# Performance work log

Hardware: AMD Instinct MI355X
Metric: run time of the kernel (lower is better)

The kernel has to match this reference:

```python
import jax, jax.numpy as jnp
import numpy as np

B, LP, LH, D, H = 32, 1024, 1024, 256, 256

def setup_inputs() -> dict:
    key = jax.random.key(0)
    k1, k2, k3 = jax.random.split(key, 3)
    premises = jax.random.normal(k1, (B, LP, D), dtype=jnp.float32)
    hypotheses = jax.random.normal(k2, (B, LH, D), dtype=jnp.float32)
    W_F = jax.random.normal(k3, (D, H), dtype=jnp.float32) * (1.0 / np.sqrt(D))
    return {"premises": premises, "hypotheses": hypotheses, "W_F": W_F}

def reference(premises, hypotheses, W_F):
    # Tanh-projected features: F_p = tanh(P @ W_F), F_h = tanh(H @ W_F)
    F_p = jnp.tanh(jnp.einsum('bpd,dh->bph', premises, W_F))   # [B,LP,H]
    F_h = jnp.tanh(jnp.einsum('bqd,dh->bqh', hypotheses, W_F)) # [B,LH,H]
    # Alignment scores e_ij = F_p . F_h
    eijs = jnp.einsum('bph,bqh->bpq', F_p, F_h)                # [B,LP,LH]
    # betas: for each premise token, softmax over hypothesis tokens, weighted sum of hypotheses
    betas = jnp.einsum('bpq,bqd->bpd', jax.nn.softmax(eijs, axis=-1), hypotheses)  # [B,LP,D]
    # alphas: for each hypothesis token, softmax over premise tokens, weighted sum of premises
    alphas = jnp.einsum('bqp,bpd->bqd',
                        jax.nn.softmax(jnp.swapaxes(eijs, 1, 2), axis=-1),
                        premises)                                                   # [B,LH,D]
    return betas, alphas
```

## Files before the change

kernel.cpp:

```cpp
#include <hip/hip_runtime.h>

typedef _Float16 f16;
typedef __attribute__((ext_vector_type(4))) _Float16 f16x4;
typedef __attribute__((ext_vector_type(8))) _Float16 f16x8;
typedef __attribute__((ext_vector_type(4))) float f32x4;
typedef __attribute__((ext_vector_type(16))) float f32x16;
typedef unsigned int u32;

#define BB 32
#define LL 1024
#define DD 256

#define VMCNT(N) asm volatile("s_waitcnt vmcnt(" #N ")" ::: "memory")
#define LGKMCNT0 asm volatile("s_waitcnt lgkmcnt(0)" ::: "memory")

__device__ __forceinline__ void async_copy16(const f16* g, f16* l) {
  __builtin_amdgcn_global_load_lds(
      (const __attribute__((address_space(1))) u32*)(const void*)g,
      (__attribute__((address_space(3))) u32*)(void*)l, 16, 0, 0);
}

__device__ __forceinline__ u32 pack_pkrtz(float a, float b) {
  auto pk = __builtin_amdgcn_cvt_pkrtz(a, b);
  u32 w;
  __builtin_memcpy(&w, &pk, 4);
  return w;
}


__global__ __launch_bounds__(256) void w_to_frag(const float* __restrict__ W,
                                                 f16* __restrict__ WtF) {
  __shared__ float T32[256][33];
  const int tid = threadIdx.x;
  const int N = blockIdx.x;
  const int nn = tid & 31, kr = tid >> 5;
#pragma unroll
  for (int p = 0; p < 32; ++p) {
    int k = p * 8 + kr;
    T32[k][nn] = W[(size_t)k * 256 + N * 32 + nn];
  }
  __syncthreads();
  const int wv = tid >> 6, lane = tid & 63;
  const int l32 = lane & 31, half = lane >> 5;
#pragma unroll
  for (int i = 0; i < 4; ++i) {
    int s = wv * 4 + i;
    f16x8 ov;
#pragma unroll
    for (int j = 0; j < 8; ++j) ov[j] = (f16)T32[s * 16 + half * 8 + j][l32];
    *(f16x8*)&WtF[(size_t)N * 8192 + s * 512 + lane * 8] = ov;
  }
}

__global__ __launch_bounds__(256, 3) void proj_mfma(
    const float* __restrict__ Pin, const float* __restrict__ Hin,
    const f16* __restrict__ WtF, f16* __restrict__ Fp, f16* __restrict__ Fh,
    f16* __restrict__ Vtp, f16* __restrict__ Vth) {
  __shared__ f16 As[64][264];
  const int tid = threadIdx.x;
  const int wv = tid >> 6, lane = tid & 63;
  const int l32 = lane & 31, half = lane >> 5;
  const int wm = wv >> 1, wn = wv & 1;
  const float* A = blockIdx.z ? Hin : Pin;
  f16* F = blockIdx.z ? Fh : Fp;
  f16* VtO = blockIdx.z ? Vth : Vtp;
  const int m0 = blockIdx.x * 64;
  const int T0 = m0 >> 5;

  {
    const int r = tid >> 4;
    const int c4 = (tid & 15) * 4;
#pragma unroll
    for (int pp = 0; pp < 4; ++pp)
#pragma unroll
      for (int ch = 0; ch < 4; ++ch) {
        float4 v =
            *(const float4*)&A[(size_t)(m0 + r + pp * 16) * 256 + ch * 64 + c4];
        f16x4 h4;
        h4[0] = (f16)v.x; h4[1] = (f16)v.y; h4[2] = (f16)v.z; h4[3] = (f16)v.w;
        *(f16x4*)&As[r + pp * 16][ch * 64 + c4] = h4;
      }
  }
  __syncthreads();

  f16x8 af[16];
#pragma unroll
  for (int ks = 0; ks < 16; ++ks)
    af[ks] = *(const f16x8*)&As[wm * 32 + l32][ks * 16 + half * 8];

  {
#pragma unroll
    for (int i = 0; i < 8; ++i) {
      int idx = wv * 8 + i;
      int Tl = idx >> 4;
      int t = (idx >> 1) & 7;
      int qh = idx & 1;
      int qb = Tl * 32 + qh * 16 + half * 8;
      f16x8 ov;
#pragma unroll
      for (int j = 0; j < 8; ++j) ov[j] = As[qb + j][t * 32 + l32];
      *(f16x8*)&VtO[(size_t)(T0 + Tl) * 8192 + t * 1024 + qh * 512 +
                    half * 256 + l32 * 8] = ov;
    }
  }
  __syncthreads();

#pragma unroll
  for (int nc = 0; nc < 4; ++nc) {
    f32x16 acc = (f32x16)(0.f);
#pragma unroll
    for (int ks = 0; ks < 16; ++ks) {
      f16x8 wf = *(const f16x8*)&WtF[(size_t)nc * 16384 + wn * 8192 +
                                     ks * 512 + lane * 8];
      acc = __builtin_amdgcn_mfma_f32_32x32x16_f16(af[ks], wf, acc, 0, 0, 0);
    }
#pragma unroll
    for (int r = 0; r < 16; ++r) {
      float xv = acc[r];
      float e2 = __expf(2.f * xv);
      float th = 1.f - 2.f / (e2 + 1.f);
      As[wm * 32 + (r & 3) + 8 * (r >> 2) + 4 * half]
        [nc * 64 + wn * 32 + l32] = (f16)th;
    }
  }
  __syncthreads();

#pragma unroll
  for (int i = 0; i < 8; ++i) {
    int idx = wv * 8 + i;
    int Tl = idx >> 4;
    int s = idx & 15;
    f16x8 ov = *(const f16x8*)&As[Tl * 32 + l32][s * 16 + half * 8];
    *(f16x8*)&F[(size_t)(T0 + Tl) * 8192 + s * 512 + half * 256 + l32 * 8] =
        ov;
  }
}

__global__ __launch_bounds__(512, 2) void flash_mfma(
    const f16* __restrict__ Fpm, const f16* __restrict__ Fhm,
    const f16* __restrict__ Vth, const f16* __restrict__ Vtp,
    float* __restrict__ Out) {
  __shared__ f16 SMEM[5][8192];

  const int tid = threadIdx.x;
  const int wv = tid >> 6, lane = tid & 63;
  const int l32 = lane & 31, half = lane >> 5;

  const f16* Fq = Fpm;
  const f16* Fk = Fhm;
  const f16* Vt = Vth;
  float* O = Out;
  if (blockIdx.y) { Fq = Fhm; Fk = Fpm; Vt = Vtp; O = Out + (size_t)BB * LL * DD; }

  const int x = blockIdx.x;
  const int b = ((x >> 5) << 3) | (x & 7);
  const int pblk = (x >> 3) & 3;
  const int p0 = pblk * 256 + wv * 32;
  const int p = p0 + l32;

  const f16* Fq_b = Fq + (size_t)b * LL * DD;
  const f16* Fk_b = Fk + (size_t)b * LL * DD;
  const f16* Vt_b = Vt + (size_t)b * LL * DD;

  f16x8 qf[16];
  {
    const f16* qt = Fq_b + (size_t)(p >> 5) * 8192 + half * 256 + (p & 31) * 8;
#pragma unroll
    for (int s = 0; s < 16; ++s) qf[s] = *(const f16x8*)&qt[s * 512];
  }

  float m_run = -1e30f, l_run = 0.f;
  f32x16 o[8];
#pragma unroll
  for (int t = 0; t < 8; ++t) o[t] = (f32x16)(0.f);

  auto stage_K = [&](int slot, int T) {
    const f16* kt = Fk_b + (size_t)T * 8192 + wv * 1024 + lane * 8;
    async_copy16(kt, &SMEM[slot][wv * 1024]);
    async_copy16(kt + 512, &SMEM[slot][wv * 1024 + 512]);
  };
  auto stage_V = [&](int slot, int T) {
    const f16* vt = Vt_b + (size_t)T * 8192 + wv * 1024 + lane * 8;
    async_copy16(vt, &SMEM[2 + slot][wv * 1024]);
    async_copy16(vt + 512, &SMEM[2 + slot][wv * 1024 + 512]);
  };

  auto qk16 = [&](int slot) {
    f32x16 S = (f32x16)(0.f);
    __builtin_amdgcn_s_setprio(1);
#pragma unroll
    for (int s = 0; s < 16; ++s) {
      f16x8 kf = *(const f16x8*)&SMEM[slot][s * 512 + lane * 8];
      S = __builtin_amdgcn_mfma_f32_32x32x16_f16(kf, qf[s], S, 0, 0, 0);
    }
    __builtin_amdgcn_s_setprio(0);
    return S;
  };

  f16x8 pf[2];
  auto softmax_pack = [&](const f32x16& S) {
    float mt = S[0];
#pragma unroll
    for (int r = 1; r < 16; ++r) mt = fmaxf(mt, S[r]);
    mt = fmaxf(mt, __shfl_xor(mt, 32, 64));
    const bool keep = __all((int)(mt - m_run <= 8.0f)) != 0;
    const float mn = keep ? m_run : fmaxf(m_run, mt);
    float pe[16];
    float ts = 0.f;
#pragma unroll
    for (int r = 0; r < 16; ++r) {
      pe[r] = __expf(S[r] - mn);
      ts += pe[r];
    }
    ts += __shfl_xor(ts, 32, 64);
    if (!keep) {
      const float alpha = __expf(m_run - mn);
      l_run *= alpha;
      m_run = mn;
#pragma unroll
      for (int t = 0; t < 8; ++t)
#pragma unroll
        for (int r = 0; r < 16; ++r) o[t][r] *= alpha;
    }
    l_run += ts;

    u32 pw[8];
#pragma unroll
    for (int i = 0; i < 8; ++i) pw[i] = pack_pkrtz(pe[2 * i], pe[2 * i + 1]);
    u32 rc[4];
    {
      u32 s0 = half ? pw[0] : pw[2];
      u32 s1 = half ? pw[1] : pw[3];
      u32 s2 = half ? pw[4] : pw[6];
      u32 s3 = half ? pw[5] : pw[7];
      rc[0] = (u32)__shfl_xor((int)s0, 32, 64);
      rc[1] = (u32)__shfl_xor((int)s1, 32, 64);
      rc[2] = (u32)__shfl_xor((int)s2, 32, 64);
      rc[3] = (u32)__shfl_xor((int)s3, 32, 64);
    }
#pragma unroll
    for (int h = 0; h < 2; ++h) {
      u32 tmp[4];
      tmp[0] = half ? rc[2 * h] : pw[4 * h];
      tmp[1] = half ? rc[2 * h + 1] : pw[4 * h + 1];
      tmp[2] = half ? pw[4 * h + 2] : rc[2 * h];
      tmp[3] = half ? pw[4 * h + 3] : rc[2 * h + 1];
      __builtin_memcpy(&pf[h], tmp, 16);
    }
  };

  auto pv = [&](int slot) {
    __builtin_amdgcn_s_setprio(1);
#pragma unroll
    for (int t = 0; t < 8; ++t) {
      f16x8 v0 = *(const f16x8*)&SMEM[2 + slot][t * 1024 + lane * 8];
      o[t] = __builtin_amdgcn_mfma_f32_32x32x16_f16(v0, pf[0], o[t], 0, 0, 0);
      f16x8 v1 = *(const f16x8*)&SMEM[2 + slot][t * 1024 + 512 + lane * 8];
      o[t] = __builtin_amdgcn_mfma_f32_32x32x16_f16(v1, pf[1], o[t], 0, 0, 0);
    }
    __builtin_amdgcn_s_setprio(0);
  };

  stage_K(0, 0);
  stage_V(0, 0);
  stage_K(1, 1);
  stage_V(1, 1);
  VMCNT(4);
  __builtin_amdgcn_sched_barrier(0);
  __builtin_amdgcn_s_barrier();
  f32x16 Scur = qk16(0);

  for (int it = 0; it < 31; ++it) {
    if (it < 30) {
      stage_K(it & 1, it + 2);
      stage_V((it + 2) % 3, it + 2);
      VMCNT(4);
    } else {
      VMCNT(0);
    }
    __builtin_amdgcn_sched_barrier(0);
    __builtin_amdgcn_s_barrier();
    f32x16 Snext = qk16((it + 1) & 1);
    softmax_pack(Scur);
    pv(it % 3);
    __builtin_amdgcn_s_barrier();
    Scur = Snext;
  }
  softmax_pack(Scur);
  pv(31 % 3);
  __syncthreads();

  const float inv = 1.f / l_run;
  float* Tw = (float*)&SMEM[0][0] + wv * (32 * 36);
  float* Ob = O + (size_t)b * LL * DD;
#pragma unroll
  for (int t = 0; t < 8; ++t) {
#pragma unroll
    for (int g = 0; g < 4; ++g) {
      int C = 2 * g + half;
      f32x4 v;
      v[0] = o[t][4 * g + 0] * inv;
      v[1] = o[t][4 * g + 1] * inv;
      v[2] = o[t][4 * g + 2] * inv;
      v[3] = o[t][4 * g + 3] * inv;
      *(f32x4*)&Tw[l32 * 36 + C * 4] = v;
    }
    LGKMCNT0;
#pragma unroll
    for (int pass = 0; pass < 4; ++pass) {
      int row = pass * 8 + (lane >> 3);
      int Cr = lane & 7;
      f32x4 v = *(const f32x4*)&Tw[row * 36 + Cr * 4];
      *(f32x4*)&Ob[(size_t)(p0 + row) * DD + t * 32 + Cr * 4] = v;
    }
    LGKMCNT0;
  }
}

extern "C" void kernel_launch(void* const* d_in, const int* in_sizes, int n_in,
                              void* d_out, int out_size, void* d_ws,
                              size_t ws_size, hipStream_t stream) {
  const float* premises = (const float*)d_in[0];
  const float* hypotheses = (const float*)d_in[1];
  const float* W = (const float*)d_in[2];
  float* out = (float*)d_out;

  const size_t MF = (size_t)BB * LL * DD;
  f16* Fp = (f16*)d_ws;
  f16* Fh = Fp + MF;
  f16* Vth = Fh + MF;
  f16* Vtp = Vth + MF;
  f16* WtF = (f16*)((char*)d_out + (size_t)out_size * 4 - 256 * 256 * 2);

  w_to_frag<<<dim3(8), 256, 0, stream>>>(W, WtF);
  proj_mfma<<<dim3(512, 1, 2), 256, 0, stream>>>(premises, hypotheses, WtF, Fp,
                                                 Fh, Vtp, Vth);
  flash_mfma<<<dim3(128, 2), 512, 0, stream>>>(Fp, Fh, Vth, Vtp, out);
}
```

Baseline: 209.6 us.

## Stream K tiles directly from global into registers instead of staging through LDS

Removes the LDS double-buffer for K tiles and has each wave load its K fragments straight from global memory into registers, using a 4-register rotating prefetch interleaved with the QK MFMAs. Only V stays staged in LDS (3 slots), which cuts LDS footprint from 5 to 3 buffers. The loop also drops the software pipeline that computed the next tile's QK while doing softmax and PV on the current one, so QK is now serial with softmax/PV. The risk is exposed global load latency, and every wave in the block redundantly fetches the same K tile from global/L2.

Measured after the change: 230.2 us. +9.8%, slower.

```diff
diff --git a/kernel.cpp b/kernel.cpp
--- a/kernel.cpp
+++ b/kernel.cpp
@@ -140,7 +140,7 @@
     const f16* __restrict__ Fpm, const f16* __restrict__ Fhm,
     const f16* __restrict__ Vth, const f16* __restrict__ Vtp,
     float* __restrict__ Out) {
-  __shared__ f16 SMEM[5][8192];
+  __shared__ f16 SMEM[3][8192];
 
   const int tid = threadIdx.x;
   const int wv = tid >> 6, lane = tid & 63;
@@ -174,27 +174,10 @@
 #pragma unroll
   for (int t = 0; t < 8; ++t) o[t] = (f32x16)(0.f);
 
-  auto stage_K = [&](int slot, int T) {
-    const f16* kt = Fk_b + (size_t)T * 8192 + wv * 1024 + lane * 8;
-    async_copy16(kt, &SMEM[slot][wv * 1024]);
-    async_copy16(kt + 512, &SMEM[slot][wv * 1024 + 512]);
-  };
   auto stage_V = [&](int slot, int T) {
     const f16* vt = Vt_b + (size_t)T * 8192 + wv * 1024 + lane * 8;
-    async_copy16(vt, &SMEM[2 + slot][wv * 1024]);
-    async_copy16(vt + 512, &SMEM[2 + slot][wv * 1024 + 512]);
-  };
-
-  auto qk16 = [&](int slot) {
-    f32x16 S = (f32x16)(0.f);
-    __builtin_amdgcn_s_setprio(1);
-#pragma unroll
-    for (int s = 0; s < 16; ++s) {
-      f16x8 kf = *(const f16x8*)&SMEM[slot][s * 512 + lane * 8];
-      S = __builtin_amdgcn_mfma_f32_32x32x16_f16(kf, qf[s], S, 0, 0, 0);
-    }
-    __builtin_amdgcn_s_setprio(0);
-    return S;
+    async_copy16(vt, &SMEM[slot][wv * 1024]);
+    async_copy16(vt + 512, &SMEM[slot][wv * 1024 + 512]);
   };
 
   f16x8 pf[2];
@@ -253,41 +236,71 @@
     __builtin_amdgcn_s_setprio(1);
 #pragma unroll
     for (int t = 0; t < 8; ++t) {
-      f16x8 v0 = *(const f16x8*)&SMEM[2 + slot][t * 1024 + lane * 8];
+      f16x8 v0 = *(const f16x8*)&SMEM[slot][t * 1024 + lane * 8];
       o[t] = __builtin_amdgcn_mfma_f32_32x32x16_f16(v0, pf[0], o[t], 0, 0, 0);
-      f16x8 v1 = *(const f16x8*)&SMEM[2 + slot][t * 1024 + 512 + lane * 8];
+      f16x8 v1 = *(const f16x8*)&SMEM[slot][t * 1024 + 512 + lane * 8];
       o[t] = __builtin_amdgcn_mfma_f32_32x32x16_f16(v1, pf[1], o[t], 0, 0, 0);
     }
     __builtin_amdgcn_s_setprio(0);
   };
 
-  stage_K(0, 0);
+#define MFMA_F16(A, B, C) __builtin_amdgcn_mfma_f32_32x32x16_f16(A, B, C, 0, 0, 0)
+
   stage_V(0, 0);
-  stage_K(1, 1);
   stage_V(1, 1);
-  VMCNT(4);
+  f16x8 ka, kb, kc, kd;
+  {
+    const f16* kt = Fk_b + lane * 8;
+    ka = *(const f16x8*)&kt[0 * 512];
+    kb = *(const f16x8*)&kt[1 * 512];
+    kc = *(const f16x8*)&kt[2 * 512];
+    kd = *(const f16x8*)&kt[3 * 512];
+  }
+  VMCNT(2);
   __builtin_amdgcn_sched_barrier(0);
   __builtin_amdgcn_s_barrier();
-  f32x16 Scur = qk16(0);
-
-  for (int it = 0; it < 31; ++it) {
-    if (it < 30) {
-      stage_K(it & 1, it + 2);
-      stage_V((it + 2) % 3, it + 2);
-      VMCNT(4);
-    } else {
-      VMCNT(0);
-    }
+
+  for (int it = 0; it < 32; ++it) {
+    if (it + 2 < 32) stage_V((it + 2) % 3, it + 2);
+    VMCNT(2);
     __builtin_amdgcn_sched_barrier(0);
+
+    f32x16 S;
+    {
+      const f16* kt = Fk_b + (size_t)it * 8192 + lane * 8;
+      S = (f32x16)(0.f);
+      __builtin_amdgcn_s_setprio(1);
+      S = MFMA_F16(ka, qf[0], S);  ka = *(const f16x8*)&kt[4 * 512];
+      S = MFMA_F16(kb, qf[1], S);  kb = *(const f16x8*)&kt[5 * 512];
+      S = MFMA_F16(kc, qf[2], S);  kc = *(const f16x8*)&kt[6 * 512];
+      S = MFMA_F16(kd, qf[3], S);  kd = *(const f16x8*)&kt[7 * 512];
+      S = MFMA_F16(ka, qf[4], S);  ka = *(const f16x8*)&kt[8 * 512];
+      S = MFMA_F16(kb, qf[5], S);  kb = *(const f16x8*)&kt[9 * 512];
+      S = MFMA_F16(kc, qf[6], S);  kc = *(const f16x8*)&kt[10 * 512];
+      S = MFMA_F16(kd, qf[7], S);  kd = *(const f16x8*)&kt[11 * 512];
+      S = MFMA_F16(ka, qf[8], S);  ka = *(const f16x8*)&kt[12 * 512];
+      S = MFMA_F16(kb, qf[9], S);  kb = *(const f16x8*)&kt[13 * 512];
+      S = MFMA_F16(kc, qf[10], S); kc = *(const f16x8*)&kt[14 * 512];
+      S = MFMA_F16(kd, qf[11], S); kd = *(const f16x8*)&kt[15 * 512];
+      S = MFMA_F16(ka, qf[12], S);
+      S = MFMA_F16(kb, qf[13], S);
+      S = MFMA_F16(kc, qf[14], S);
+      S = MFMA_F16(kd, qf[15], S);
+      __builtin_amdgcn_s_setprio(0);
+    }
+
+    softmax_pack(S);
+    pv(it % 3);
+
+    if (it < 31) {
+      const f16* kn = Fk_b + (size_t)(it + 1) * 8192 + lane * 8;
+      ka = *(const f16x8*)&kn[0 * 512];
+      kb = *(const f16x8*)&kn[1 * 512];
+      kc = *(const f16x8*)&kn[2 * 512];
+      kd = *(const f16x8*)&kn[3 * 512];
+    }
     __builtin_amdgcn_s_barrier();
-    f32x16 Snext = qk16((it + 1) & 1);
-    softmax_pack(Scur);
-    pv(it % 3);
-    __builtin_amdgcn_s_barrier();
-    Scur = Snext;
-  }
-  softmax_pack(Scur);
-  pv(31 % 3);
+  }
   __syncthreads();
 
   const float inv = 1.f / l_run;
```
